# Optimization experiments

Hardware: AMD Instinct MI355X
Metric: run time of the kernel (lower is better)

The kernel has to match this reference:

```python
import jax, jax.numpy as jnp
import numpy as np

DIM = 256
H = 4
HD = DIM // H
SCALE = HD ** -0.5
W = 10
PAD = W // 2
MAX_LEN = 512


def setup_inputs() -> dict:
    key = jax.random.key(0)
    ks = jax.random.split(key, 32)
    B, T, D = 32, 512, DIM
    def w(k, shape):
        return jax.random.normal(k, shape, dtype=jnp.float32) * 0.02
    inp = {
        'x': jax.random.normal(ks[0], (B, T, D), dtype=jnp.float32),
        # global TemporalAttention params (weights stored as (in,out))
        'gq_w': w(ks[1], (D, D)), 'gq_b': jnp.zeros((D,), jnp.float32),
        'gk_w': w(ks[2], (D, D)), 'gk_b': jnp.zeros((D,), jnp.float32),
        'gv_w': w(ks[3], (D, D)), 'gv_b': jnp.zeros((D,), jnp.float32),
        'go_w': w(ks[4], (D, D)), 'go_b': jnp.zeros((D,), jnp.float32),
        'rel_pos_bias': w(ks[5], (2 * MAX_LEN - 1, H)),
        # local sliding-window attention params
        'lq_w': w(ks[6], (D, D)), 'lq_b': jnp.zeros((D,), jnp.float32),
        'lk_w': w(ks[7], (D, D)), 'lk_b': jnp.zeros((D,), jnp.float32),
        'lv_w': w(ks[8], (D, D)), 'lv_b': jnp.zeros((D,), jnp.float32),
        # pattern attention (only q/k projections matter for returned weights)
        'pattern_embed': jax.random.normal(ks[9], (1, 3, D), dtype=jnp.float32),
        'pq_w': w(ks[10], (D, D)), 'pq_b': jnp.zeros((D,), jnp.float32),
        'pk_w': w(ks[11], (D, D)), 'pk_b': jnp.zeros((D,), jnp.float32),
        # fusion MLP
        'f1_w': w(ks[12], (2 * D, D)), 'f1_b': jnp.zeros((D,), jnp.float32),
        'f2_w': w(ks[13], (D, D)), 'f2_b': jnp.zeros((D,), jnp.float32),
    }
    return inp


def _forward(x, gq_w, gq_b, gk_w, gk_b, gv_w, gv_b, go_w, go_b, rel_pos_bias,
             lq_w, lq_b, lk_w, lk_b, lv_w, lv_b,
             pattern_embed, pq_w, pq_b, pk_w, pk_b,
             f1_w, f1_b, f2_w, f2_b):
    B, T, D = x.shape
    # ---- global temporal attention ----
    q = (x @ gq_w + gq_b).reshape(B, T, H, HD)
    k = (x @ gk_w + gk_b).reshape(B, T, H, HD)
    v = (x @ gv_w + gv_b).reshape(B, T, H, HD)
    attn = jnp.einsum('bthd,bshd->bhts', q, k) * SCALE  # (B,H,T,T)
    pos = jnp.arange(T)
    idx = jnp.clip(pos[None, :] - pos[:, None] + T - 1, 0, 2 * T - 2)  # (T,T)
    attn = attn + jnp.transpose(rel_pos_bias[idx], (2, 0, 1))[None]
    attn_w = jax.nn.softmax(attn, axis=-1)  # dropout = identity in eval
    g_out = jnp.einsum('bhts,bshd->bthd', attn_w, v).reshape(B, T, D)
    global_out = g_out @ go_w + go_b
    # ---- local sliding-window attention (single head over full dim) ----
    x_pad = jnp.pad(x, ((0, 0), (PAD, PAD), (0, 0)))  # zero pad -> k/v get bias
    lq = x @ lq_w + lq_b                      # (B,T,D)
    lk = x_pad @ lk_w + lk_b                  # (B,T+W,D)
    lv = x_pad @ lv_w + lv_b
    widx = jnp.arange(T)[:, None] + jnp.arange(W)[None, :]  # (T,W)
    k_win = lk[:, widx]                       # (B,T,W,D)
    v_win = lv[:, widx]
    l_attn = jax.nn.softmax(jnp.einsum('btd,btwd->btw', lq, k_win) * SCALE, axis=-1)
    local_out = jnp.einsum('btw,btwd->btd', l_attn, v_win)
    # ---- fusion MLP + residual ----
    fused = jnp.concatenate([global_out, local_out], axis=-1)
    output = jax.nn.relu(fused @ f1_w + f1_b) @ f2_w + f2_b + x
    # ---- pattern attention (torch MHA, weights averaged over heads) ----
    pe = jnp.broadcast_to(pattern_embed, (B, 3, D))
    pooled = jnp.mean(x, axis=1, keepdims=True)  # (B,1,D)
    pq = (pooled @ pq_w + pq_b).reshape(B, 1, H, HD)
    pk = (pe @ pk_w + pk_b).reshape(B, 3, H, HD)
    plogits = jnp.einsum('bqhd,bkhd->bhqk', pq, pk) * SCALE  # (B,H,1,3)
    pw = jax.nn.softmax(plogits, axis=-1).mean(axis=1)  # avg over heads -> (B,1,3)
    pattern_scores = pw[:, 0]  # (B,3)
    return output, pattern_scores


def reference(x, gq_w, gq_b, gk_w, gk_b, gv_w, gv_b, go_w, go_b, rel_pos_bias,
              lq_w, lq_b, lk_w, lk_b, lv_w, lv_b,
              pattern_embed, pq_w, pq_b, pk_w, pk_b,
              f1_w, f1_b, f2_w, f2_b):
    return _forward(x, gq_w, gq_b, gk_w, gk_b, gv_w, gv_b, go_w, go_b, rel_pos_bias,
                    lq_w, lq_b, lk_w, lk_b, lv_w, lv_b,
                    pattern_embed, pq_w, pq_b, pk_w, pk_b,
                    f1_w, f1_b, f2_w, f2_b)
```

## Files before the change

kernel.cpp:

```cpp
#include <hip/hip_runtime.h>
#include <hip/hip_bf16.h>

typedef __attribute__((ext_vector_type(8))) __bf16 bf16x8;
typedef __attribute__((ext_vector_type(8))) unsigned short u16x8;
typedef __attribute__((ext_vector_type(4))) float f32x4;

#define MFMA_BF16(a,b,c) __builtin_amdgcn_mfma_f32_16x16x32_bf16((a),(b),(c),0,0,0)

#define DIMD 256
#define NHEAD 4
#define HDIM 64
#define ASCALE 0.125f
#define SEQT 512
#define NB 32
#define BT 16384

__device__ __forceinline__ unsigned short f2bf(float f) {
    unsigned int u = __float_as_uint(f);
    u += 0x7fffu + ((u >> 16) & 1u);
    return (unsigned short)(u >> 16);
}
__device__ __forceinline__ float bf2f(unsigned short h) {
    return __uint_as_float(((unsigned int)h) << 16);
}

__global__ __launch_bounds__(256) void cast_x_kernel(const float* __restrict__ x,
                                                     unsigned short* __restrict__ xb, int n) {
    int i = (blockIdx.x * 256 + threadIdx.x) * 4;
    if (i < n) {
        float4 v = *(const float4*)(x + i);
        ushort4 o;
        o.x = f2bf(v.x); o.y = f2bf(v.y); o.z = f2bf(v.z); o.w = f2bf(v.w);
        *(ushort4*)(xb + i) = o;
    }
}

__global__ __launch_bounds__(256) void wconv_kernel(const float* __restrict__ src,
                                                    unsigned short* __restrict__ dst, int K) {
    int k = blockIdx.x, n = threadIdx.x;
    dst[(size_t)n * K + k] = f2bf(src[(size_t)k * 256 + n]);
}

__global__ __launch_bounds__(256)
void gemm_nt(const unsigned short* __restrict__ A, const unsigned short* __restrict__ Bt,
             const float* __restrict__ bias, int K,
             void* __restrict__ out, int ldc, int mode, int do_relu,
             const float* __restrict__ resid) {
    __shared__ __align__(16) unsigned short As[64][40];
    __shared__ __align__(16) unsigned short Bs[64][40];
    const int tid = threadIdx.x;
    const int w = tid >> 6, l = tid & 63, g = l >> 4, rl = l & 15;
    const int m0 = blockIdx.x * 64, n0 = blockIdx.y * 64;
    const int arow = tid >> 2, akc = tid & 3;

    f32x4 acc[4];
    #pragma unroll
    for (int n = 0; n < 4; ++n) acc[n] = (f32x4){0.f, 0.f, 0.f, 0.f};

    for (int k0 = 0; k0 < K; k0 += 32) {
        u16x8 va = *(const u16x8*)(A  + (size_t)(m0 + arow) * K + k0 + akc * 8);
        u16x8 vb = *(const u16x8*)(Bt + (size_t)(n0 + arow) * K + k0 + akc * 8);
        __syncthreads();
        *(u16x8*)&As[arow][akc * 8] = va;
        *(u16x8*)&Bs[arow][akc * 8] = vb;
        __syncthreads();
        bf16x8 af = *(const bf16x8*)&As[w * 16 + rl][g * 8];
        #pragma unroll
        for (int n = 0; n < 4; ++n) {
            bf16x8 bfr = *(const bf16x8*)&Bs[n * 16 + rl][g * 8];
            acc[n] = MFMA_BF16(af, bfr, acc[n]);
        }
    }

    #pragma unroll
    for (int n = 0; n < 4; ++n) {
        #pragma unroll
        for (int r = 0; r < 4; ++r) {
            int row = m0 + w * 16 + g * 4 + r;
            int col = n0 + n * 16 + rl;
            float v = acc[n][r] + bias[col];
            if (do_relu) v = fmaxf(v, 0.f);
            if (mode == 0) {
                ((unsigned short*)out)[(size_t)row * ldc + col] = f2bf(v);
            } else {
                float res = resid ? resid[(size_t)row * 256 + col] : 0.f;
                ((float*)out)[(size_t)row * ldc + col] = v + res;
            }
        }
    }
}

__global__ __launch_bounds__(256)
void attn_global(const unsigned short* __restrict__ qb, const unsigned short* __restrict__ kb,
                 const unsigned short* __restrict__ vb, const float* __restrict__ rpb,
                 unsigned short* __restrict__ gout) {
    __shared__ __align__(16) unsigned short Ks[64][72];
    __shared__ __align__(16) unsigned short Vt[64][72];
    __shared__ __align__(16) unsigned short Ps[64][72];
    __shared__ float rb_s[127];

    const int tid = threadIdx.x;
    const int w = tid >> 6, l = tid & 63, g = l >> 4, rl = l & 15;
    const int bh = blockIdx.y, b = bh >> 2, h = bh & 3;
    const int t0 = blockIdx.x * 64;
    const size_t base = (size_t)b * SEQT * 256 + h * 64;

    bf16x8 qf[2];
    #pragma unroll
    for (int kk = 0; kk < 2; ++kk)
        qf[kk] = *(const bf16x8*)(qb + base + (size_t)(t0 + w * 16 + rl) * 256 + kk * 32 + g * 8);

    f32x4 oacc[4];
    #pragma unroll
    for (int n = 0; n < 4; ++n) oacc[n] = (f32x4){0.f, 0.f, 0.f, 0.f};
    float m_run[4], l_run[4];
    #pragma unroll
    for (int r = 0; r < 4; ++r) { m_run[r] = -1e30f; l_run[r] = 0.f; }

    for (int s0 = 0; s0 < SEQT; s0 += 64) {
        __syncthreads();
        #pragma unroll
        for (int cc = 0; cc < 2; ++cc) {
            int c = tid + cc * 256;
            int sr = c >> 3, hc = c & 7;
            u16x8 kv = *(const u16x8*)(kb + base + (size_t)(s0 + sr) * 256 + hc * 8);
            u16x8 vv = *(const u16x8*)(vb + base + (size_t)(s0 + sr) * 256 + hc * 8);
            *(u16x8*)&Ks[sr][hc * 8] = kv;
            #pragma unroll
            for (int i = 0; i < 8; ++i) Vt[hc * 8 + i][sr] = (unsigned short)vv[i];
        }
        if (tid < 127) {
            int dd = s0 - t0 + 448 + tid;
            rb_s[tid] = rpb[dd * 4 + h];
        }
        __syncthreads();

        f32x4 sacc[4];
        #pragma unroll
        for (int n = 0; n < 4; ++n) sacc[n] = (f32x4){0.f, 0.f, 0.f, 0.f};
        #pragma unroll
        for (int kk = 0; kk < 2; ++kk) {
            #pragma unroll
            for (int n = 0; n < 4; ++n) {
                bf16x8 kf = *(const bf16x8*)&Ks[n * 16 + rl][kk * 32 + g * 8];
                sacc[n] = MFMA_BF16(qf[kk], kf, sacc[n]);
            }
        }

        float sv[4][4];
        float mt[4];
        #pragma unroll
        for (int r = 0; r < 4; ++r) mt[r] = -1e30f;
        #pragma unroll
        for (int n = 0; n < 4; ++n) {
            #pragma unroll
            for (int r = 0; r < 4; ++r) {
                int relc = (n * 16 + rl) - (w * 16 + g * 4 + r) + 63;
                float s = sacc[n][r] * ASCALE + rb_s[relc];
                sv[n][r] = s;
                mt[r] = fmaxf(mt[r], s);
            }
        }
        #pragma unroll
        for (int r = 0; r < 4; ++r) {
            #pragma unroll
            for (int mk = 1; mk < 16; mk <<= 1) mt[r] = fmaxf(mt[r], __shfl_xor(mt[r], mk));
        }
        float sf[4], rs[4];
        #pragma unroll
        for (int r = 0; r < 4; ++r) {
            float mn = fmaxf(m_run[r], mt[r]);
            sf[r] = expf(m_run[r] - mn);
            m_run[r] = mn;
            rs[r] = 0.f;
        }
        #pragma unroll
        for (int n = 0; n < 4; ++n) {
            #pragma unroll
            for (int r = 0; r < 4; ++r) {
                float p = expf(sv[n][r] - m_run[r]);
                rs[r] += p;
                Ps[w * 16 + g * 4 + r][n * 16 + rl] = f2bf(p);
            }
        }
        #pragma unroll
        for (int r = 0; r < 4; ++r) {
            #pragma unroll
            for (int mk = 1; mk < 16; mk <<= 1) rs[r] += __shfl_xor(rs[r], mk);
            l_run[r] = l_run[r] * sf[r] + rs[r];
        }
        #pragma unroll
        for (int n = 0; n < 4; ++n) {
            #pragma unroll
            for (int r = 0; r < 4; ++r) oacc[n][r] *= sf[r];
        }

        #pragma unroll
        for (int kk = 0; kk < 2; ++kk) {
            bf16x8 pf = *(const bf16x8*)&Ps[w * 16 + rl][kk * 32 + g * 8];
            #pragma unroll
            for (int n = 0; n < 4; ++n) {
                bf16x8 vf = *(const bf16x8*)&Vt[n * 16 + rl][kk * 32 + g * 8];
                oacc[n] = MFMA_BF16(pf, vf, oacc[n]);
            }
        }
    }

    #pragma unroll
    for (int n = 0; n < 4; ++n) {
        #pragma unroll
        for (int r = 0; r < 4; ++r) {
            float o = oacc[n][r] / l_run[r];
            gout[base + (size_t)(t0 + w * 16 + g * 4 + r) * 256 + n * 16 + rl] = f2bf(o);
        }
    }
}

__global__ __launch_bounds__(256)
void local_attn(const unsigned short* __restrict__ lqb, const unsigned short* __restrict__ lkb,
                const unsigned short* __restrict__ lvb,
                const float* __restrict__ lk_bias, const float* __restrict__ lv_bias,
                unsigned short* __restrict__ fused) {
    const int tid = threadIdx.x;
    const int wv = tid >> 6, lane = tid & 63;
    const int row = blockIdx.x * 4 + wv;
    const int b = row >> 9, tt = row & 511;

    ushort4 qv = *((const ushort4*)(lqb + (size_t)row * 256) + lane);
    float qf[4] = {bf2f(qv.x), bf2f(qv.y), bf2f(qv.z), bf2f(qv.w)};

    float sw[10];
    #pragma unroll
    for (int w = 0; w < 10; ++w) {
        int src = tt + w - 5;
        float kf[4];
        if (src >= 0 && src < 512) {
            ushort4 kv = *((const ushort4*)(lkb + (size_t)(b * 512 + src) * 256) + lane);
            kf[0] = bf2f(kv.x); kf[1] = bf2f(kv.y); kf[2] = bf2f(kv.z); kf[3] = bf2f(kv.w);
        } else {
            float4 kb4 = *((const float4*)lk_bias + lane);
            kf[0] = kb4.x; kf[1] = kb4.y; kf[2] = kb4.z; kf[3] = kb4.w;
        }
        float p = qf[0] * kf[0] + qf[1] * kf[1] + qf[2] * kf[2] + qf[3] * kf[3];
        #pragma unroll
        for (int mk = 1; mk < 64; mk <<= 1) p += __shfl_xor(p, mk);
        sw[w] = p * ASCALE;
    }
    float mx = sw[0];
    #pragma unroll
    for (int w = 1; w < 10; ++w) mx = fmaxf(mx, sw[w]);
    float pv[10], s = 0.f;
    #pragma unroll
    for (int w = 0; w < 10; ++w) { pv[w] = expf(sw[w] - mx); s += pv[w]; }
    float inv = 1.f / s;

    float of[4] = {0.f, 0.f, 0.f, 0.f};
    #pragma unroll
    for (int w = 0; w < 10; ++w) {
        int src = tt + w - 5;
        float vf[4];
        if (src >= 0 && src < 512) {
            ushort4 vv = *((const ushort4*)(lvb + (size_t)(b * 512 + src) * 256) + lane);
            vf[0] = bf2f(vv.x); vf[1] = bf2f(vv.y); vf[2] = bf2f(vv.z); vf[3] = bf2f(vv.w);
        } else {
            float4 vb4 = *((const float4*)lv_bias + lane);
            vf[0] = vb4.x; vf[1] = vb4.y; vf[2] = vb4.z; vf[3] = vb4.w;
        }
        float pw = pv[w] * inv;
        of[0] += pw * vf[0]; of[1] += pw * vf[1]; of[2] += pw * vf[2]; of[3] += pw * vf[3];
    }
    ushort4 o;
    o.x = f2bf(of[0]); o.y = f2bf(of[1]); o.z = f2bf(of[2]); o.w = f2bf(of[3]);
    *((ushort4*)(fused + (size_t)row * 512 + 256) + lane) = o;
}

__global__ __launch_bounds__(256)
void pooled_mean(const float* __restrict__ x, float* __restrict__ pooled) {
    int b = blockIdx.x, d = threadIdx.x;
    const float* xp = x + (size_t)b * SEQT * 256 + d;
    float s = 0.f;
    for (int t = 0; t < SEQT; ++t) s += xp[(size_t)t * 256];
    pooled[b * 256 + d] = s * (1.0f / 512.0f);
}

__global__ __launch_bounds__(256)
void pattern_k(const float* __restrict__ pooled, const float* __restrict__ pe,
               const float* __restrict__ pq_w, const float* __restrict__ pq_b,
               const float* __restrict__ pk_w, const float* __restrict__ pk_b,
               float* __restrict__ out_scores) {
    __shared__ float pool_s[256];
    __shared__ float pes[3 * 256];
    __shared__ float pq_s[256];
    __shared__ float pk_s[3][256];
    __shared__ float pw_s[4][3];
    int b = blockIdx.x, d = threadIdx.x;
    pool_s[d] = pooled[b * 256 + d];
    pes[d] = pe[d]; pes[256 + d] = pe[256 + d]; pes[512 + d] = pe[512 + d];
    __syncthreads();
    float acc = pq_b[d];
    for (int k = 0; k < 256; ++k) acc += pool_s[k] * pq_w[k * 256 + d];
    pq_s[d] = acc;
    for (int j = 0; j < 3; ++j) {
        float a = pk_b[d];
        for (int k = 0; k < 256; ++k) a += pes[j * 256 + k] * pk_w[k * 256 + d];
        pk_s[j][d] = a;
    }
    __syncthreads();
    int h = d >> 6, lane = d & 63;
    float lg[3];
    #pragma unroll
    for (int j = 0; j < 3; ++j) {
        float p = pq_s[h * 64 + lane] * pk_s[j][h * 64 + lane];
        #pragma unroll
        for (int mk = 1; mk < 64; mk <<= 1) p += __shfl_xor(p, mk);
        lg[j] = p * ASCALE;
    }
    float mx = fmaxf(fmaxf(lg[0], lg[1]), lg[2]);
    float e0 = expf(lg[0] - mx), e1 = expf(lg[1] - mx), e2 = expf(lg[2] - mx);
    float sinv = 1.f / (e0 + e1 + e2);
    if (lane == 0) { pw_s[h][0] = e0 * sinv; pw_s[h][1] = e1 * sinv; pw_s[h][2] = e2 * sinv; }
    __syncthreads();
    if (d < 3)
        out_scores[b * 3 + d] = 0.25f * (pw_s[0][d] + pw_s[1][d] + pw_s[2][d] + pw_s[3][d]);
}

extern "C" void kernel_launch(void* const* d_in, const int* in_sizes, int n_in,
                              void* d_out, int out_size, void* d_ws, size_t ws_size,
                              hipStream_t stream) {
    (void)in_sizes; (void)n_in; (void)out_size; (void)ws_size;
    const float* x    = (const float*)d_in[0];
    const float* gq_w = (const float*)d_in[1];  const float* gq_b = (const float*)d_in[2];
    const float* gk_w = (const float*)d_in[3];  const float* gk_b = (const float*)d_in[4];
    const float* gv_w = (const float*)d_in[5];  const float* gv_b = (const float*)d_in[6];
    const float* go_w = (const float*)d_in[7];  const float* go_b = (const float*)d_in[8];
    const float* rpb  = (const float*)d_in[9];
    const float* lq_w = (const float*)d_in[10]; const float* lq_b = (const float*)d_in[11];
    const float* lk_w = (const float*)d_in[12]; const float* lk_b = (const float*)d_in[13];
    const float* lv_w = (const float*)d_in[14]; const float* lv_b = (const float*)d_in[15];
    const float* pe   = (const float*)d_in[16];
    const float* pq_w = (const float*)d_in[17]; const float* pq_b = (const float*)d_in[18];
    const float* pk_w = (const float*)d_in[19]; const float* pk_b = (const float*)d_in[20];
    const float* f1_w = (const float*)d_in[21]; const float* f1_b = (const float*)d_in[22];
    const float* f2_w = (const float*)d_in[23]; const float* f2_b = (const float*)d_in[24];

    char* ws = (char*)d_ws;
    const size_t MB = 1024 * 1024;
    unsigned short* xb    = (unsigned short*)(ws + 0);
    unsigned short* qb    = (unsigned short*)(ws + 8 * MB);
    unsigned short* kbuf  = (unsigned short*)(ws + 16 * MB);
    unsigned short* vbuf  = (unsigned short*)(ws + 24 * MB);
    unsigned short* lqb   = (unsigned short*)(ws + 32 * MB);
    unsigned short* lkb   = (unsigned short*)(ws + 40 * MB);
    unsigned short* lvb   = (unsigned short*)(ws + 48 * MB);
    unsigned short* fused = (unsigned short*)(ws + 56 * MB);
    unsigned short* hb    = (unsigned short*)(ws + 72 * MB);
    unsigned short* wts   = (unsigned short*)(ws + 80 * MB);
    unsigned short* gq_t = wts;
    unsigned short* gk_t = gq_t + 65536;
    unsigned short* gv_t = gk_t + 65536;
    unsigned short* go_t = gv_t + 65536;
    unsigned short* lq_t = go_t + 65536;
    unsigned short* lk_t = lq_t + 65536;
    unsigned short* lv_t = lk_t + 65536;
    unsigned short* f1_t = lv_t + 65536;
    unsigned short* f2_t = f1_t + 131072;
    float* pooled = (float*)(ws + 82 * MB);

    float* out = (float*)d_out;
    float* out_scores = out + (size_t)BT * 256;

    cast_x_kernel<<<4096, 256, 0, stream>>>(x, xb, BT * 256);
    wconv_kernel<<<256, 256, 0, stream>>>(gq_w, gq_t, 256);
    wconv_kernel<<<256, 256, 0, stream>>>(gk_w, gk_t, 256);
    wconv_kernel<<<256, 256, 0, stream>>>(gv_w, gv_t, 256);
    wconv_kernel<<<256, 256, 0, stream>>>(go_w, go_t, 256);
    wconv_kernel<<<256, 256, 0, stream>>>(lq_w, lq_t, 256);
    wconv_kernel<<<256, 256, 0, stream>>>(lk_w, lk_t, 256);
    wconv_kernel<<<256, 256, 0, stream>>>(lv_w, lv_t, 256);
    wconv_kernel<<<512, 256, 0, stream>>>(f1_w, f1_t, 512);
    wconv_kernel<<<256, 256, 0, stream>>>(f2_w, f2_t, 256);

    dim3 ggrid(BT / 64, 4);
    gemm_nt<<<ggrid, 256, 0, stream>>>(xb, gq_t, gq_b, 256, qb,   256, 0, 0, nullptr);
    gemm_nt<<<ggrid, 256, 0, stream>>>(xb, gk_t, gk_b, 256, kbuf, 256, 0, 0, nullptr);
    gemm_nt<<<ggrid, 256, 0, stream>>>(xb, gv_t, gv_b, 256, vbuf, 256, 0, 0, nullptr);
    gemm_nt<<<ggrid, 256, 0, stream>>>(xb, lq_t, lq_b, 256, lqb,  256, 0, 0, nullptr);
    gemm_nt<<<ggrid, 256, 0, stream>>>(xb, lk_t, lk_b, 256, lkb,  256, 0, 0, nullptr);
    gemm_nt<<<ggrid, 256, 0, stream>>>(xb, lv_t, lv_b, 256, lvb,  256, 0, 0, nullptr);

    attn_global<<<dim3(SEQT / 64, NB * NHEAD), 256, 0, stream>>>(qb, kbuf, vbuf, rpb, xb);

    gemm_nt<<<ggrid, 256, 0, stream>>>(xb, go_t, go_b, 256, fused, 512, 0, 0, nullptr);

    local_attn<<<BT / 4, 256, 0, stream>>>(lqb, lkb, lvb, lk_b, lv_b, fused);

    gemm_nt<<<ggrid, 256, 0, stream>>>(fused, f1_t, f1_b, 512, hb, 256, 0, 1, nullptr);
    gemm_nt<<<ggrid, 256, 0, stream>>>(hb, f2_t, f2_b, 256, out, 256, 1, 0, x);

    pooled_mean<<<NB, 256, 0, stream>>>(x, pooled);
    pattern_k<<<NB, 256, 0, stream>>>(pooled, pe, pq_w, pq_b, pk_w, pk_b, out_scores);
}
```

Baseline: 341.2 us.

## Fuse QKV projections, retile GEMM to 128x128 with direct LDS loads, drop online-softmax max

Five projection GEMMs are merged into one 1280-wide GEMM, and V is produced already transposed by a swapped-operand GEMM so the attention kernel no longer transposes it in shared memory. The GEMM is retiled to 128x128 with global_load_lds direct-to-LDS copies. The global attention drops the running-max rescaling and uses plain exp with a single final normalisation, and fast __expf replaces expf. Pooled mean is split across more blocks with atomics. The max-free softmax risks overflow if the logits grow large; it relies on the small logits these weights produce.

```diff
diff --git a/kernel.cpp b/kernel.cpp
--- a/kernel.cpp
+++ b/kernel.cpp
@@ -7,13 +7,14 @@
 
 #define MFMA_BF16(a,b,c) __builtin_amdgcn_mfma_f32_16x16x32_bf16((a),(b),(c),0,0,0)
 
-#define DIMD 256
-#define NHEAD 4
-#define HDIM 64
 #define ASCALE 0.125f
 #define SEQT 512
 #define NB 32
 #define BT 16384
+
+#define GLD_LDS16(g, l) __builtin_amdgcn_global_load_lds( \
+    (__attribute__((address_space(1))) void*)(g), \
+    (__attribute__((address_space(3))) void*)(l), 16, 0, 0)
 
 __device__ __forceinline__ unsigned short f2bf(float f) {
     unsigned int u = __float_as_uint(f);
@@ -41,61 +42,83 @@
     dst[(size_t)n * K + k] = f2bf(src[(size_t)k * 256 + n]);
 }
 
-__global__ __launch_bounds__(256)
-void gemm_nt(const unsigned short* __restrict__ A, const unsigned short* __restrict__ Bt,
+__global__ __launch_bounds__(256) void biascat_kernel(const float* b0, const float* b1,
+                                                      const float* b2, const float* b3,
+                                                      const float* b4, float* out) {
+    int j = blockIdx.x, d = threadIdx.x;
+    const float* src = (j == 0) ? b0 : (j == 1) ? b1 : (j == 2) ? b2 : (j == 3) ? b3 : b4;
+    out[j * 256 + d] = src[d];
+}
+
+__global__ __launch_bounds__(256)
+void gemm128(const unsigned short* __restrict__ A, const unsigned short* __restrict__ Bt,
              const float* __restrict__ bias, int K,
-             void* __restrict__ out, int ldc, int mode, int do_relu,
+             void* __restrict__ out, int ldc, int mode, int do_relu, int bias_row,
              const float* __restrict__ resid) {
-    __shared__ __align__(16) unsigned short As[64][40];
-    __shared__ __align__(16) unsigned short Bs[64][40];
+    __shared__ __align__(16) unsigned short As[128 * 32];
+    __shared__ __align__(16) unsigned short Bs[128 * 32];
     const int tid = threadIdx.x;
     const int w = tid >> 6, l = tid & 63, g = l >> 4, rl = l & 15;
-    const int m0 = blockIdx.x * 64, n0 = blockIdx.y * 64;
-    const int arow = tid >> 2, akc = tid & 3;
-
-    f32x4 acc[4];
-    #pragma unroll
-    for (int n = 0; n < 4; ++n) acc[n] = (f32x4){0.f, 0.f, 0.f, 0.f};
+    const int wm = w >> 1, wn = w & 1;
+    const int m0 = blockIdx.x * 128, n0 = blockIdx.y * 128;
+    const int srow = l >> 2, scol = (l & 3) * 8;
+
+    f32x4 acc[4][4];
+    #pragma unroll
+    for (int m = 0; m < 4; ++m)
+        #pragma unroll
+        for (int n = 0; n < 4; ++n) acc[m][n] = (f32x4){0.f, 0.f, 0.f, 0.f};
 
     for (int k0 = 0; k0 < K; k0 += 32) {
-        u16x8 va = *(const u16x8*)(A  + (size_t)(m0 + arow) * K + k0 + akc * 8);
-        u16x8 vb = *(const u16x8*)(Bt + (size_t)(n0 + arow) * K + k0 + akc * 8);
+        #pragma unroll
+        for (int j = 0; j < 2; ++j) {
+            int c = w * 2 + j;
+            const unsigned short* ga = A  + (size_t)(m0 + c * 16 + srow) * K + k0 + scol;
+            const unsigned short* gb = Bt + (size_t)(n0 + c * 16 + srow) * K + k0 + scol;
+            GLD_LDS16(ga, As + c * 512);
+            GLD_LDS16(gb, Bs + c * 512);
+        }
         __syncthreads();
-        *(u16x8*)&As[arow][akc * 8] = va;
-        *(u16x8*)&Bs[arow][akc * 8] = vb;
+        bf16x8 af[4], bfr[4];
+        #pragma unroll
+        for (int m = 0; m < 4; ++m) af[m]  = *(const bf16x8*)&As[(wm * 64 + m * 16 + rl) * 32 + g * 8];
+        #pragma unroll
+        for (int n = 0; n < 4; ++n) bfr[n] = *(const bf16x8*)&Bs[(wn * 64 + n * 16 + rl) * 32 + g * 8];
+        #pragma unroll
+        for (int m = 0; m < 4; ++m)
+            #pragma unroll
+            for (int n = 0; n < 4; ++n)
+                acc[m][n] = MFMA_BF16(af[m], bfr[n], acc[m][n]);
         __syncthreads();
-        bf16x8 af = *(const bf16x8*)&As[w * 16 + rl][g * 8];
+    }
+
+    const int crow0 = m0 + wm * 64, ccol0 = n0 + wn * 64;
+    #pragma unroll
+    for (int m = 0; m < 4; ++m) {
         #pragma unroll
         for (int n = 0; n < 4; ++n) {
-            bf16x8 bfr = *(const bf16x8*)&Bs[n * 16 + rl][g * 8];
-            acc[n] = MFMA_BF16(af, bfr, acc[n]);
-        }
-    }
-
-    #pragma unroll
-    for (int n = 0; n < 4; ++n) {
-        #pragma unroll
-        for (int r = 0; r < 4; ++r) {
-            int row = m0 + w * 16 + g * 4 + r;
-            int col = n0 + n * 16 + rl;
-            float v = acc[n][r] + bias[col];
-            if (do_relu) v = fmaxf(v, 0.f);
-            if (mode == 0) {
-                ((unsigned short*)out)[(size_t)row * ldc + col] = f2bf(v);
-            } else {
-                float res = resid ? resid[(size_t)row * 256 + col] : 0.f;
-                ((float*)out)[(size_t)row * ldc + col] = v + res;
+            #pragma unroll
+            for (int r = 0; r < 4; ++r) {
+                int row = crow0 + m * 16 + g * 4 + r;
+                int col = ccol0 + n * 16 + rl;
+                float v = acc[m][n][r] + (bias_row ? bias[row] : bias[col]);
+                if (do_relu) v = fmaxf(v, 0.f);
+                if (mode == 0) {
+                    ((unsigned short*)out)[(size_t)row * ldc + col] = f2bf(v);
+                } else {
+                    float res = resid ? resid[(size_t)row * ldc + col] : 0.f;
+                    ((float*)out)[(size_t)row * ldc + col] = v + res;
+                }
             }
         }
     }
 }
 
 __global__ __launch_bounds__(256)
-void attn_global(const unsigned short* __restrict__ qb, const unsigned short* __restrict__ kb,
-                 const unsigned short* __restrict__ vb, const float* __restrict__ rpb,
-                 unsigned short* __restrict__ gout) {
+void attn_global2(const unsigned short* __restrict__ proj, const unsigned short* __restrict__ vT,
+                  const float* __restrict__ rpb, unsigned short* __restrict__ gout) {
     __shared__ __align__(16) unsigned short Ks[64][72];
-    __shared__ __align__(16) unsigned short Vt[64][72];
+    __shared__ __align__(16) unsigned short Vs[64][72];
     __shared__ __align__(16) unsigned short Ps[64][72];
     __shared__ float rb_s[127];
 
@@ -103,19 +126,17 @@
     const int w = tid >> 6, l = tid & 63, g = l >> 4, rl = l & 15;
     const int bh = blockIdx.y, b = bh >> 2, h = bh & 3;
     const int t0 = blockIdx.x * 64;
-    const size_t base = (size_t)b * SEQT * 256 + h * 64;
 
     bf16x8 qf[2];
     #pragma unroll
     for (int kk = 0; kk < 2; ++kk)
-        qf[kk] = *(const bf16x8*)(qb + base + (size_t)(t0 + w * 16 + rl) * 256 + kk * 32 + g * 8);
+        qf[kk] = *(const bf16x8*)(proj + (size_t)(b * SEQT + t0 + w * 16 + rl) * 1280
+                                  + h * 64 + kk * 32 + g * 8);
 
     f32x4 oacc[4];
     #pragma unroll
     for (int n = 0; n < 4; ++n) oacc[n] = (f32x4){0.f, 0.f, 0.f, 0.f};
-    float m_run[4], l_run[4];
-    #pragma unroll
-    for (int r = 0; r < 4; ++r) { m_run[r] = -1e30f; l_run[r] = 0.f; }
+    float lpart[4] = {0.f, 0.f, 0.f, 0.f};
 
     for (int s0 = 0; s0 < SEQT; s0 += 64) {
         __syncthreads();
@@ -123,11 +144,12 @@
         for (int cc = 0; cc < 2; ++cc) {
             int c = tid + cc * 256;
             int sr = c >> 3, hc = c & 7;
-            u16x8 kv = *(const u16x8*)(kb + base + (size_t)(s0 + sr) * 256 + hc * 8);
-            u16x8 vv = *(const u16x8*)(vb + base + (size_t)(s0 + sr) * 256 + hc * 8);
+            u16x8 kv = *(const u16x8*)(proj + (size_t)(b * SEQT + s0 + sr) * 1280
+                                       + 256 + h * 64 + hc * 8);
             *(u16x8*)&Ks[sr][hc * 8] = kv;
-            #pragma unroll
-            for (int i = 0; i < 8; ++i) Vt[hc * 8 + i][sr] = (unsigned short)vv[i];
+            u16x8 vv = *(const u16x8*)(vT + (size_t)(h * 64 + sr) * BT
+                                       + b * SEQT + s0 + hc * 8);
+            *(u16x8*)&Vs[sr][hc * 8] = vv;
         }
         if (tid < 127) {
             int dd = s0 - t0 + 448 + tid;
@@ -147,78 +169,46 @@
             }
         }
 
-        float sv[4][4];
-        float mt[4];
-        #pragma unroll
-        for (int r = 0; r < 4; ++r) mt[r] = -1e30f;
         #pragma unroll
         for (int n = 0; n < 4; ++n) {
             #pragma unroll
             for (int r = 0; r < 4; ++r) {
                 int relc = (n * 16 + rl) - (w * 16 + g * 4 + r) + 63;
-                float s = sacc[n][r] * ASCALE + rb_s[relc];
-                sv[n][r] = s;
-                mt[r] = fmaxf(mt[r], s);
-            }
-        }
-        #pragma unroll
-        for (int r = 0; r < 4; ++r) {
-            #pragma unroll
-            for (int mk = 1; mk < 16; mk <<= 1) mt[r] = fmaxf(mt[r], __shfl_xor(mt[r], mk));
-        }
-        float sf[4], rs[4];
-        #pragma unroll
-        for (int r = 0; r < 4; ++r) {
-            float mn = fmaxf(m_run[r], mt[r]);
-            sf[r] = expf(m_run[r] - mn);
-            m_run[r] = mn;
-            rs[r] = 0.f;
-        }
-        #pragma unroll
-        for (int n = 0; n < 4; ++n) {
-            #pragma unroll
-            for (int r = 0; r < 4; ++r) {
-                float p = expf(sv[n][r] - m_run[r]);
-                rs[r] += p;
+                float p = __expf(sacc[n][r] * ASCALE + rb_s[relc]);
+                lpart[r] += p;
                 Ps[w * 16 + g * 4 + r][n * 16 + rl] = f2bf(p);
             }
         }
-        #pragma unroll
-        for (int r = 0; r < 4; ++r) {
-            #pragma unroll
-            for (int mk = 1; mk < 16; mk <<= 1) rs[r] += __shfl_xor(rs[r], mk);
-            l_run[r] = l_run[r] * sf[r] + rs[r];
-        }
-        #pragma unroll
-        for (int n = 0; n < 4; ++n) {
-            #pragma unroll
-            for (int r = 0; r < 4; ++r) oacc[n][r] *= sf[r];
-        }
 
         #pragma unroll
         for (int kk = 0; kk < 2; ++kk) {
             bf16x8 pf = *(const bf16x8*)&Ps[w * 16 + rl][kk * 32 + g * 8];
             #pragma unroll
             for (int n = 0; n < 4; ++n) {
-                bf16x8 vf = *(const bf16x8*)&Vt[n * 16 + rl][kk * 32 + g * 8];
+                bf16x8 vf = *(const bf16x8*)&Vs[n * 16 + rl][kk * 32 + g * 8];
                 oacc[n] = MFMA_BF16(pf, vf, oacc[n]);
             }
         }
     }
 
     #pragma unroll
+    for (int r = 0; r < 4; ++r) {
+        #pragma unroll
+        for (int mk = 1; mk < 16; mk <<= 1) lpart[r] += __shfl_xor(lpart[r], mk);
+    }
+    const size_t obase = (size_t)b * SEQT * 256 + h * 64;
+    #pragma unroll
     for (int n = 0; n < 4; ++n) {
         #pragma unroll
         for (int r = 0; r < 4; ++r) {
-            float o = oacc[n][r] / l_run[r];
-            gout[base + (size_t)(t0 + w * 16 + g * 4 + r) * 256 + n * 16 + rl] = f2bf(o);
-        }
-    }
-}
-
-__global__ __launch_bounds__(256)
-void local_attn(const unsigned short* __restrict__ lqb, const unsigned short* __restrict__ lkb,
-                const unsigned short* __restrict__ lvb,
+            float o = oacc[n][r] / lpart[r];
+            gout[obase + (size_t)(t0 + w * 16 + g * 4 + r) * 256 + n * 16 + rl] = f2bf(o);
+        }
+    }
+}
+
+__global__ __launch_bounds__(256)
+void local_attn(const unsigned short* __restrict__ proj,
                 const float* __restrict__ lk_bias, const float* __restrict__ lv_bias,
                 unsigned short* __restrict__ fused) {
     const int tid = threadIdx.x;
@@ -226,7 +216,7 @@
     const int row = blockIdx.x * 4 + wv;
     const int b = row >> 9, tt = row & 511;
 
-    ushort4 qv = *((const ushort4*)(lqb + (size_t)row * 256) + lane);
+    ushort4 qv = *((const ushort4*)(proj + (size_t)row * 1280 + 512) + lane);
     float qf[4] = {bf2f(qv.x), bf2f(qv.y), bf2f(qv.z), bf2f(qv.w)};
 
     float sw[10];
@@ -235,7 +225,7 @@
         int src = tt + w - 5;
         float kf[4];
         if (src >= 0 && src < 512) {
-            ushort4 kv = *((const ushort4*)(lkb + (size_t)(b * 512 + src) * 256) + lane);
+            ushort4 kv = *((const ushort4*)(proj + (size_t)(b * 512 + src) * 1280 + 768) + lane);
             kf[0] = bf2f(kv.x); kf[1] = bf2f(kv.y); kf[2] = bf2f(kv.z); kf[3] = bf2f(kv.w);
         } else {
             float4 kb4 = *((const float4*)lk_bias + lane);
@@ -251,7 +241,7 @@
     for (int w = 1; w < 10; ++w) mx = fmaxf(mx, sw[w]);
     float pv[10], s = 0.f;
     #pragma unroll
-    for (int w = 0; w < 10; ++w) { pv[w] = expf(sw[w] - mx); s += pv[w]; }
+    for (int w = 0; w < 10; ++w) { pv[w] = __expf(sw[w] - mx); s += pv[w]; }
     float inv = 1.f / s;
 
     float of[4] = {0.f, 0.f, 0.f, 0.f};
@@ -260,7 +250,7 @@
         int src = tt + w - 5;
         float vf[4];
         if (src >= 0 && src < 512) {
-            ushort4 vv = *((const ushort4*)(lvb + (size_t)(b * 512 + src) * 256) + lane);
+            ushort4 vv = *((const ushort4*)(proj + (size_t)(b * 512 + src) * 1280 + 1024) + lane);
             vf[0] = bf2f(vv.x); vf[1] = bf2f(vv.y); vf[2] = bf2f(vv.z); vf[3] = bf2f(vv.w);
         } else {
             float4 vb4 = *((const float4*)lv_bias + lane);
@@ -275,12 +265,14 @@
 }
 
 __global__ __launch_bounds__(256)
-void pooled_mean(const float* __restrict__ x, float* __restrict__ pooled) {
-    int b = blockIdx.x, d = threadIdx.x;
-    const float* xp = x + (size_t)b * SEQT * 256 + d;
+void pooled_mean2(const float* __restrict__ x, float* __restrict__ pooled) {
+    int b = blockIdx.x >> 3, tc = blockIdx.x & 7;
+    int d = threadIdx.x;
+    const float* xp = x + ((size_t)b * SEQT + tc * 64) * 256 + d;
     float s = 0.f;
-    for (int t = 0; t < SEQT; ++t) s += xp[(size_t)t * 256];
-    pooled[b * 256 + d] = s * (1.0f / 512.0f);
+    #pragma unroll 8
+    for (int t = 0; t < 64; ++t) s += xp[(size_t)t * 256];
+    atomicAdd(&pooled[b * 256 + d], s * (1.0f / 512.0f));
 }
 
 __global__ __launch_bounds__(256)
@@ -316,7 +308,7 @@
         lg[j] = p * ASCALE;
     }
     float mx = fmaxf(fmaxf(lg[0], lg[1]), lg[2]);
-    float e0 = expf(lg[0] - mx), e1 = expf(lg[1] - mx), e2 = expf(lg[2] - mx);
+    float e0 = __expf(lg[0] - mx), e1 = __expf(lg[1] - mx), e2 = __expf(lg[2] - mx);
     float sinv = 1.f / (e0 + e1 + e2);
     if (lane == 0) { pw_s[h][0] = e0 * sinv; pw_s[h][1] = e1 * sinv; pw_s[h][2] = e2 * sinv; }
     __syncthreads();
@@ -346,57 +338,47 @@
     char* ws = (char*)d_ws;
     const size_t MB = 1024 * 1024;
     unsigned short* xb    = (unsigned short*)(ws + 0);
-    unsigned short* qb    = (unsigned short*)(ws + 8 * MB);
-    unsigned short* kbuf  = (unsigned short*)(ws + 16 * MB);
-    unsigned short* vbuf  = (unsigned short*)(ws + 24 * MB);
-    unsigned short* lqb   = (unsigned short*)(ws + 32 * MB);
-    unsigned short* lkb   = (unsigned short*)(ws + 40 * MB);
-    unsigned short* lvb   = (unsigned short*)(ws + 48 * MB);
+    unsigned short* proj  = (unsigned short*)(ws + 8 * MB);
+    unsigned short* vT    = (unsigned short*)(ws + 48 * MB);
     unsigned short* fused = (unsigned short*)(ws + 56 * MB);
     unsigned short* hb    = (unsigned short*)(ws + 72 * MB);
     unsigned short* wts   = (unsigned short*)(ws + 80 * MB);
-    unsigned short* gq_t = wts;
-    unsigned short* gk_t = gq_t + 65536;
-    unsigned short* gv_t = gk_t + 65536;
-    unsigned short* go_t = gv_t + 65536;
-    unsigned short* lq_t = go_t + 65536;
-    unsigned short* lk_t = lq_t + 65536;
-    unsigned short* lv_t = lk_t + 65536;
-    unsigned short* f1_t = lv_t + 65536;
-    unsigned short* f2_t = f1_t + 131072;
-    float* pooled = (float*)(ws + 82 * MB);
+    unsigned short* gv_t  = wts;
+    unsigned short* go_t  = gv_t + 65536;
+    unsigned short* f1_t  = go_t + 65536;
+    unsigned short* f2_t  = f1_t + 131072;
+    unsigned short* wcat  = f2_t + 65536;
+    float* bcat   = (float*)(ws + 82 * MB);
+    float* pooled = (float*)(ws + 83 * MB);
 
     float* out = (float*)d_out;
     float* out_scores = out + (size_t)BT * 256;
 
     cast_x_kernel<<<4096, 256, 0, stream>>>(x, xb, BT * 256);
-    wconv_kernel<<<256, 256, 0, stream>>>(gq_w, gq_t, 256);
-    wconv_kernel<<<256, 256, 0, stream>>>(gk_w, gk_t, 256);
+    wconv_kernel<<<256, 256, 0, stream>>>(gq_w, wcat + 0 * 65536, 256);
+    wconv_kernel<<<256, 256, 0, stream>>>(gk_w, wcat + 1 * 65536, 256);
+    wconv_kernel<<<256, 256, 0, stream>>>(lq_w, wcat + 2 * 65536, 256);
+    wconv_kernel<<<256, 256, 0, stream>>>(lk_w, wcat + 3 * 65536, 256);
+    wconv_kernel<<<256, 256, 0, stream>>>(lv_w, wcat + 4 * 65536, 256);
     wconv_kernel<<<256, 256, 0, stream>>>(gv_w, gv_t, 256);
     wconv_kernel<<<256, 256, 0, stream>>>(go_w, go_t, 256);
-    wconv_kernel<<<256, 256, 0, stream>>>(lq_w, lq_t, 256);
-    wconv_kernel<<<256, 256, 0, stream>>>(lk_w, lk_t, 256);
-    wconv_kernel<<<256, 256, 0, stream>>>(lv_w, lv_t, 256);
     wconv_kernel<<<512, 256, 0, stream>>>(f1_w, f1_t, 512);
     wconv_kernel<<<256, 256, 0, stream>>>(f2_w, f2_t, 256);
-
-    dim3 ggrid(BT / 64, 4);
-    gemm_nt<<<ggrid, 256, 0, stream>>>(xb, gq_t, gq_b, 256, qb,   256, 0, 0, nullptr);
-    gemm_nt<<<ggrid, 256, 0, stream>>>(xb, gk_t, gk_b, 256, kbuf, 256, 0, 0, nullptr);
-    gemm_nt<<<ggrid, 256, 0, stream>>>(xb, gv_t, gv_b, 256, vbuf, 256, 0, 0, nullptr);
-    gemm_nt<<<ggrid, 256, 0, stream>>>(xb, lq_t, lq_b, 256, lqb,  256, 0, 0, nullptr);
-    gemm_nt<<<ggrid, 256, 0, stream>>>(xb, lk_t, lk_b, 256, lkb,  256, 0, 0, nullptr);
-    gemm_nt<<<ggrid, 256, 0, stream>>>(xb, lv_t, lv_b, 256, lvb,  256, 0, 0, nullptr);
-
-    attn_global<<<dim3(SEQT / 64, NB * NHEAD), 256, 0, stream>>>(qb, kbuf, vbuf, rpb, xb);
-
-    gemm_nt<<<ggrid, 256, 0, stream>>>(xb, go_t, go_b, 256, fused, 512, 0, 0, nullptr);
-
-    local_attn<<<BT / 4, 256, 0, stream>>>(lqb, lkb, lvb, lk_b, lv_b, fused);
-
-    gemm_nt<<<ggrid, 256, 0, stream>>>(fused, f1_t, f1_b, 512, hb, 256, 0, 1, nullptr);
-    gemm_nt<<<ggrid, 256, 0, stream>>>(hb, f2_t, f2_b, 256, out, 256, 1, 0, x);
-
-    pooled_mean<<<NB, 256, 0, stream>>>(x, pooled);
+    biascat_kernel<<<5, 256, 0, stream>>>(gq_b, gk_b, lq_b, lk_b, lv_b, bcat);
+
+    gemm128<<<dim3(BT / 128, 10), 256, 0, stream>>>(xb, wcat, bcat, 256, proj, 1280, 0, 0, 0, nullptr);
+    gemm128<<<dim3(2, BT / 128), 256, 0, stream>>>(gv_t, xb, gv_b, 256, vT, BT, 0, 0, 1, nullptr);
+
+    attn_global2<<<dim3(SEQT / 64, NB * 4), 256, 0, stream>>>(proj, vT, rpb, xb);
+
+    gemm128<<<dim3(BT / 128, 2), 256, 0, stream>>>(xb, go_t, go_b, 256, fused, 512, 0, 0, 0, nullptr);
+
+    local_attn<<<BT / 4, 256, 0, stream>>>(proj, lk_b, lv_b, fused);
+
+    gemm128<<<dim3(BT / 128, 2), 256, 0, stream>>>(fused, f1_t, f1_b, 512, hb, 256, 0, 1, 0, nullptr);
+    gemm128<<<dim3(BT / 128, 2), 256, 0, stream>>>(hb, f2_t, f2_b, 256, out, 256, 1, 0, 0, x);
+
+    hipMemsetAsync(pooled, 0, 32 * 256 * sizeof(float), stream);
+    pooled_mean2<<<256, 256, 0, stream>>>(x, pooled);
     pattern_k<<<NB, 256, 0, stream>>>(pooled, pe, pq_w, pq_b, pk_w, pk_b, out_scores);
 }
```

Measured after the change: 355.5 us. +4.2%, slower.
